# Kernel optimization log

Measured on AMD Instinct MI355X. Metric: run time of the kernel, lower is better.

Reference implementation:

```python
import jax, jax.numpy as jnp
import numpy as np

N_HEAD = 16
WINDOW = 128
CAUSAL = False


def setup_inputs() -> dict:
    key = jax.random.key(0)
    ks = jax.random.split(key, 5)
    B, T, D = 1, 4096, 1024
    x = jax.random.normal(ks[0], (B, T, D), dtype=jnp.float32)
    w_in = jax.random.normal(ks[1], (3 * D, D), dtype=jnp.float32) * 0.02
    b_in = jax.random.normal(ks[2], (3 * D,), dtype=jnp.float32) * 0.02
    w_out = jax.random.normal(ks[3], (D, D), dtype=jnp.float32) * 0.02
    b_out = jax.random.normal(ks[4], (D,), dtype=jnp.float32) * 0.02
    return {"x": x, "w_in": w_in, "b_in": b_in, "w_out": w_out, "b_out": b_out}


def _window_attention(x, w_in, b_in, w_out, b_out):
    B, T, D = x.shape
    H = N_HEAD
    hd = D // H
    scale = 1.0 / jnp.sqrt(jnp.float32(hd))

    # fused in-projection, as in torch nn.MultiheadAttention (y = x @ W^T + b)
    qkv = jnp.einsum('btd,ed->bte', x, w_in) + b_in  # (B, T, 3D)
    q, k, v = jnp.split(qkv, 3, axis=-1)
    # (B, H, T, hd)
    q = q.reshape(B, T, H, hd).transpose(0, 2, 1, 3)
    k = k.reshape(B, T, H, hd).transpose(0, 2, 1, 3)
    v = v.reshape(B, T, H, hd).transpose(0, 2, 1, 3)

    scores = jnp.einsum('bhqd,bhkd->bhqk', q, k) * scale  # (B, H, T, T)

    idx = jnp.arange(T)
    diff = idx[:, None] - idx[None, :]
    if CAUSAL:
        allowed = (diff >= 0) & (diff <= WINDOW)
    else:
        allowed = jnp.abs(diff) <= WINDOW
    NEG = jnp.float32(-1e30)
    scores = jnp.where(allowed[None, None, :, :], scores, NEG)

    attn = jax.nn.softmax(scores, axis=-1)
    ctx = jnp.einsum('bhqk,bhkd->bhqd', attn, v)  # (B, H, T, hd)
    ctx = ctx.transpose(0, 2, 1, 3).reshape(B, T, D)
    out = jnp.einsum('btd,ed->bte', ctx, w_out) + b_out
    return x + out  # residual, as in the module


def reference(x, w_in, b_in, w_out, b_out):
    return _window_attention(x, w_in, b_in, w_out, b_out)
```

## Files before the change

### kernel.cpp

```cpp
#include <hip/hip_runtime.h>

#define T_SEQ 4096
#define DMODEL 1024
#define NHEAD 16
#define HDIM 64
#define WIN 128

typedef __attribute__((ext_vector_type(8))) short bf16x8;
typedef __attribute__((ext_vector_type(4))) float f32x4;
typedef __attribute__((ext_vector_type(4))) unsigned short u16x4;

__device__ __forceinline__ unsigned short f2bf(float f) {
  unsigned int u = __builtin_bit_cast(unsigned int, f);
  return (unsigned short)((u + 0x7fffu + ((u >> 16) & 1u)) >> 16);
}

__device__ __forceinline__ void gload_lds16(const unsigned short* g,
                                            unsigned short* l) {
  __builtin_amdgcn_global_load_lds(
      (const __attribute__((address_space(1))) void*)g,
      (__attribute__((address_space(3))) void*)l, 16, 0, 0);
}

__global__ void convert_all(const float* __restrict__ x,
                            const float* __restrict__ w_in,
                            const float* __restrict__ w_out,
                            unsigned short* __restrict__ x_bf,
                            unsigned short* __restrict__ w_in_bf,
                            unsigned short* __restrict__ w_out_bf) {
  int stride = gridDim.x * blockDim.x;
  int t0 = blockIdx.x * blockDim.x + threadIdx.x;
#define CVT(SRC, DST, N4)                                          \
  for (int i = t0; i < (N4); i += stride) {                        \
    float4 v = reinterpret_cast<const float4*>(SRC)[i];            \
    u16x4 o;                                                       \
    o.x = f2bf(v.x); o.y = f2bf(v.y); o.z = f2bf(v.z); o.w = f2bf(v.w); \
    reinterpret_cast<u16x4*>(DST)[i] = o;                          \
  }
  CVT(x, x_bf, T_SEQ * DMODEL / 4)
  CVT(w_in, w_in_bf, 3 * DMODEL * DMODEL / 4)
  CVT(w_out, w_out_bf, DMODEL * DMODEL / 4)
#undef CVT
}

template <int EPI, int BM, int BN>
__device__ __forceinline__ void gemm_body(
    const unsigned short* __restrict__ A,
    const unsigned short* __restrict__ B,
    const float* __restrict__ bias,
    unsigned short* __restrict__ q_buf,
    unsigned short* __restrict__ k_buf,
    unsigned short* __restrict__ vt_buf,
    const float* __restrict__ x_res,
    float* __restrict__ out) {
  const int K = DMODEL;
  constexpr int NT = DMODEL / 64;
  constexpr int SM = BM / 2, SN = BN / 2;
  constexpr int MR = SM / 16, NR = SN / 16;
  constexpr int AL = BM / 32, BL = BN / 32;
  __shared__ __align__(16) unsigned short As[2 * BM * 64];
  __shared__ __align__(16) unsigned short Bs[2 * BN * 64];

  int tid = threadIdx.x;
  int lane = tid & 63, wave = tid >> 6;
  int wr = wave >> 1, wc = wave & 1;
  int lo = lane & 15, hi = lane >> 4;
  int t0 = blockIdx.y * BM, e0 = blockIdx.x * BN;

  f32x4 acc[MR][NR];
#pragma unroll
  for (int m = 0; m < MR; ++m)
#pragma unroll
    for (int n = 0; n < NR; ++n) acc[m][n] = (f32x4){0.f, 0.f, 0.f, 0.f};

  int c8 = (tid & 7) ^ ((tid >> 3) & 7);
  int srow = tid >> 3;
  const unsigned short* AbaseG = A + (size_t)(t0 + srow) * K + c8 * 8;
  const unsigned short* BbaseG = B + (size_t)(e0 + srow) * K + c8 * 8;
  unsigned short* ldsAu = As + wave * 512;
  unsigned short* ldsBu = Bs + wave * 512;

  auto stage = [&](int tt) {
    int k0 = tt * 64;
    int ab = (tt & 1) * (BM * 64);
    int bb = (tt & 1) * (BN * 64);
#pragma unroll
    for (int l = 0; l < AL; ++l)
      gload_lds16(AbaseG + (size_t)l * 32 * K + k0, ldsAu + l * 2048 + ab);
#pragma unroll
    for (int l = 0; l < BL; ++l)
      gload_lds16(BbaseG + (size_t)l * 32 * K + k0, ldsBu + l * 2048 + bb);
  };

  stage(0);
  asm volatile("s_waitcnt vmcnt(0) lgkmcnt(0)\n\ts_barrier" ::: "memory");

  for (int t = 0; t < NT; ++t) {
    if (t + 1 < NT) stage(t + 1);
    const unsigned short* Ab = As + (t & 1) * (BM * 64);
    const unsigned short* Bb = Bs + (t & 1) * (BN * 64);
    bf16x8 af[MR][2], bfr[NR][2];
#pragma unroll
    for (int m = 0; m < MR; ++m) {
      int row = wr * SM + m * 16 + lo;
#pragma unroll
      for (int ks = 0; ks < 2; ++ks)
        af[m][ks] = *reinterpret_cast<const bf16x8*>(
            &Ab[row * 64 + (((ks << 2) + hi) ^ (row & 7)) * 8]);
    }
#pragma unroll
    for (int n = 0; n < NR; ++n) {
      int row = wc * SN + n * 16 + lo;
#pragma unroll
      for (int ks = 0; ks < 2; ++ks)
        bfr[n][ks] = *reinterpret_cast<const bf16x8*>(
            &Bb[row * 64 + (((ks << 2) + hi) ^ (row & 7)) * 8]);
    }
#pragma unroll
    for (int ks = 0; ks < 2; ++ks)
#pragma unroll
      for (int m = 0; m < MR; ++m)
#pragma unroll
        for (int n = 0; n < NR; ++n)
          acc[m][n] = __builtin_amdgcn_mfma_f32_16x16x32_bf16(af[m][ks], bfr[n][ks],
                                                              acc[m][n], 0, 0, 0);
    asm volatile("s_waitcnt vmcnt(0) lgkmcnt(0)\n\ts_barrier" ::: "memory");
  }

  int t0w = t0 + wr * SM;
  int e0w = e0 + wc * SN;
#pragma unroll
  for (int m = 0; m < MR; ++m) {
#pragma unroll
    for (int n = 0; n < NR; ++n) {
      int e = e0w + n * 16 + lo;
      float bv = bias[e];
      if (EPI == 0) {
        int part = e >> 10;
        int h = (e >> 6) & 15;
        int d = e & 63;
        if (part == 2) {
          int t = t0w + m * 16 + hi * 4;
          u16x4 pk;
          pk.x = f2bf(acc[m][n][0] + bv);
          pk.y = f2bf(acc[m][n][1] + bv);
          pk.z = f2bf(acc[m][n][2] + bv);
          pk.w = f2bf(acc[m][n][3] + bv);
          *reinterpret_cast<u16x4*>(&vt_buf[((size_t)(h * HDIM + d)) * T_SEQ + t]) = pk;
        } else {
          unsigned short* dst = (part == 0) ? q_buf : k_buf;
#pragma unroll
          for (int jj = 0; jj < 4; ++jj) {
            int t = t0w + m * 16 + hi * 4 + jj;
            dst[((size_t)h * T_SEQ + t) * HDIM + d] = f2bf(acc[m][n][jj] + bv);
          }
        }
      } else {
#pragma unroll
        for (int jj = 0; jj < 4; ++jj) {
          int t = t0w + m * 16 + hi * 4 + jj;
          size_t idxo = (size_t)t * DMODEL + e;
          out[idxo] = acc[m][n][jj] + bv + x_res[idxo];
        }
      }
    }
  }
}

__global__ __launch_bounds__(256) void qkv_gemm(
    const unsigned short* __restrict__ A, const unsigned short* __restrict__ B,
    const float* __restrict__ bias, unsigned short* __restrict__ q_buf,
    unsigned short* __restrict__ k_buf, unsigned short* __restrict__ vt_buf) {
  gemm_body<0, 128, 192>(A, B, bias, q_buf, k_buf, vt_buf, nullptr, nullptr);
}

__global__ __launch_bounds__(256) void out_gemm(
    const unsigned short* __restrict__ A, const unsigned short* __restrict__ B,
    const float* __restrict__ bias, const float* __restrict__ x_res,
    float* __restrict__ out) {
  gemm_body<1, 128, 64>(A, B, bias, nullptr, nullptr, nullptr, x_res, out);
}

__global__ __launch_bounds__(256) void win_attn(
    const unsigned short* __restrict__ q_buf,
    const unsigned short* __restrict__ k_buf,
    const unsigned short* __restrict__ vt_buf,
    unsigned short* __restrict__ ctx) {
  __shared__ __align__(16) unsigned short p_lds[4][2][16 * 72];
  int tid = threadIdx.x;
  int wave = tid >> 6;
  int lane = tid & 63;
  int lo = lane & 15, hi = lane >> 4;

  int id = blockIdx.x;
  int sw = (id & 7) * (512 / 8) + (id >> 3);
  int job = sw * 4 + wave;
  int h = job >> 7;
  int q0 = (job & 127) * 32;
  const float SC = 0.18033688011112042f;

  bf16x8 aq[2][2];
#pragma unroll
  for (int u = 0; u < 2; ++u) {
    const unsigned short* qrow =
        q_buf + ((size_t)h * T_SEQ + q0 + u * 16 + lo) * HDIM + hi * 8;
    aq[u][0] = *reinterpret_cast<const bf16x8*>(qrow);
    aq[u][1] = *reinterpret_cast<const bf16x8*>(qrow + 32);
  }

  float L[2][4] = {{0.f, 0.f, 0.f, 0.f}, {0.f, 0.f, 0.f, 0.f}};
  f32x4 o[2][4];
#pragma unroll
  for (int u = 0; u < 2; ++u)
#pragma unroll
    for (int n = 0; n < 4; ++n) o[u][n] = (f32x4){0.f, 0.f, 0.f, 0.f};

  int jstart = q0 - WIN; if (jstart < 0) jstart = 0;
  int jend = q0 + 32 + WIN; if (jend > T_SEQ) jend = T_SEQ;

  for (int j0 = jstart; j0 < jend; j0 += 64) {
    bf16x8 kc[4][2];
#pragma unroll
    for (int c = 0; c < 4; ++c) {
      int krow = j0 + c * 16 + lo;
      if (krow > T_SEQ - 1) krow = T_SEQ - 1;
      const unsigned short* kp = k_buf + ((size_t)h * T_SEQ + krow) * HDIM + hi * 8;
      kc[c][0] = *reinterpret_cast<const bf16x8*>(kp);
      kc[c][1] = *reinterpret_cast<const bf16x8*>(kp + 32);
    }
    bf16x8 vc[4][2];
#pragma unroll
    for (int n = 0; n < 4; ++n) {
      const unsigned short* vp =
          vt_buf + ((size_t)(h * HDIM + n * 16 + lo)) * T_SEQ + j0 + hi * 8;
      vc[n][0] = *reinterpret_cast<const bf16x8*>(vp);
      vc[n][1] = *reinterpret_cast<const bf16x8*>(vp + 32);
    }
#pragma unroll
    for (int u = 0; u < 2; ++u) {
      f32x4 z[4];
      __builtin_amdgcn_s_setprio(1);
#pragma unroll
      for (int c = 0; c < 4; ++c) {
        z[c] = (f32x4){0.f, 0.f, 0.f, 0.f};
        z[c] = __builtin_amdgcn_mfma_f32_16x16x32_bf16(aq[u][0], kc[c][0], z[c], 0, 0, 0);
        z[c] = __builtin_amdgcn_mfma_f32_16x16x32_bf16(aq[u][1], kc[c][1], z[c], 0, 0, 0);
      }
      __builtin_amdgcn_s_setprio(0);
#pragma unroll
      for (int c = 0; c < 4; ++c) {
        int kj = j0 + c * 16 + lo;
#pragma unroll
        for (int jq = 0; jq < 4; ++jq) {
          int q = q0 + u * 16 + hi * 4 + jq;
          bool ok = (q - kj <= WIN) && (kj - q <= WIN);
          float p = ok ? __builtin_amdgcn_exp2f(z[c][jq] * SC) : 0.f;
          L[u][jq] += p;
          p_lds[wave][u][(hi * 4 + jq) * 72 + c * 16 + lo] = f2bf(p);
        }
      }
    }
    bf16x8 pa[2][2];
#pragma unroll
    for (int u = 0; u < 2; ++u) {
      pa[u][0] = *reinterpret_cast<const bf16x8*>(&p_lds[wave][u][lo * 72 + hi * 8]);
      pa[u][1] = *reinterpret_cast<const bf16x8*>(&p_lds[wave][u][lo * 72 + 32 + hi * 8]);
    }
    __builtin_amdgcn_s_setprio(1);
#pragma unroll
    for (int n = 0; n < 4; ++n) {
#pragma unroll
      for (int u = 0; u < 2; ++u) {
        o[u][n] = __builtin_amdgcn_mfma_f32_16x16x32_bf16(pa[u][0], vc[n][0], o[u][n], 0, 0, 0);
        o[u][n] = __builtin_amdgcn_mfma_f32_16x16x32_bf16(pa[u][1], vc[n][1], o[u][n], 0, 0, 0);
      }
    }
    __builtin_amdgcn_s_setprio(0);
  }
#pragma unroll
  for (int u = 0; u < 2; ++u)
#pragma unroll
    for (int jq = 0; jq < 4; ++jq) {
#pragma unroll
      for (int w = 1; w < 16; w <<= 1) L[u][jq] += __shfl_xor(L[u][jq], w, 64);
    }
#pragma unroll
  for (int u = 0; u < 2; ++u)
#pragma unroll
    for (int jq = 0; jq < 4; ++jq) {
      int t = q0 + u * 16 + hi * 4 + jq;
      float inv = 1.f / L[u][jq];
#pragma unroll
      for (int n = 0; n < 4; ++n)
        ctx[(size_t)t * DMODEL + h * HDIM + n * 16 + lo] = f2bf(o[u][n][jq] * inv);
    }
}

extern "C" void kernel_launch(void* const* d_in, const int* in_sizes, int n_in,
                              void* d_out, int out_size, void* d_ws, size_t ws_size,
                              hipStream_t stream) {
  const float* x = (const float*)d_in[0];
  const float* w_in = (const float*)d_in[1];
  const float* b_in = (const float*)d_in[2];
  const float* w_out = (const float*)d_in[3];
  const float* b_out = (const float*)d_in[4];
  float* out = (float*)d_out;

  char* ws = (char*)d_ws;
  size_t off = 0;
  auto take = [&](size_t bytes) {
    char* p = ws + off;
    off += (bytes + 255) & ~(size_t)255;
    return p;
  };
  unsigned short* x_bf = (unsigned short*)take((size_t)T_SEQ * DMODEL * 2);
  unsigned short* w_in_bf = (unsigned short*)take((size_t)3 * DMODEL * DMODEL * 2);
  unsigned short* w_out_bf = (unsigned short*)take((size_t)DMODEL * DMODEL * 2);
  unsigned short* q_buf = (unsigned short*)take((size_t)T_SEQ * DMODEL * 2);
  unsigned short* k_buf = (unsigned short*)take((size_t)T_SEQ * DMODEL * 2);
  unsigned short* vt_buf = (unsigned short*)take((size_t)T_SEQ * DMODEL * 2 + 16384);
  unsigned short* ctx = (unsigned short*)take((size_t)T_SEQ * DMODEL * 2);

  convert_all<<<2048, 256, 0, stream>>>(x, w_in, w_out, x_bf, w_in_bf, w_out_bf);

  dim3 g1(3 * DMODEL / 192, T_SEQ / 128);
  qkv_gemm<<<g1, 256, 0, stream>>>(x_bf, w_in_bf, b_in, q_buf, k_buf, vt_buf);

  win_attn<<<512, 256, 0, stream>>>(q_buf, k_buf, vt_buf, ctx);

  dim3 g2(DMODEL / 64, T_SEQ / 128);
  out_gemm<<<g2, 256, 0, stream>>>(ctx, w_out_bf, b_out, x, out);
}
```

Baseline: 91.55 us.

## Widen window-attention query tile to 64 and narrow key step to 32

Each wave now handles 64 queries instead of 32, and keys are stepped 32 at a time instead of 64. The wider query tile reuses each K/V load across more queries and cuts the redundant out-of-window key work per query, since the key span per query drops from 320 to 320/64 per row. The grid is halved to 256 blocks, which lowers the number of resident waves on a 256-CU part and could leave CUs idle. Register pressure also rises from the larger accumulator set, and launch_bounds(256,1) is added to allow it.

```diff
diff --git a/kernel.cpp b/kernel.cpp
--- a/kernel.cpp
+++ b/kernel.cpp
@@ -181,74 +181,74 @@
   gemm_body<1, 128, 64>(A, B, bias, nullptr, nullptr, nullptr, x_res, out);
 }
 
-__global__ __launch_bounds__(256) void win_attn(
+__global__ __launch_bounds__(256, 1) void win_attn(
     const unsigned short* __restrict__ q_buf,
     const unsigned short* __restrict__ k_buf,
     const unsigned short* __restrict__ vt_buf,
     unsigned short* __restrict__ ctx) {
-  __shared__ __align__(16) unsigned short p_lds[4][2][16 * 72];
+  __shared__ __align__(16) unsigned short p_lds[4][4][16 * 40];
   int tid = threadIdx.x;
   int wave = tid >> 6;
   int lane = tid & 63;
   int lo = lane & 15, hi = lane >> 4;
 
   int id = blockIdx.x;
-  int sw = (id & 7) * (512 / 8) + (id >> 3);
+  int sw = (id & 7) * 32 + (id >> 3);
   int job = sw * 4 + wave;
-  int h = job >> 7;
-  int q0 = (job & 127) * 32;
+  int h = job >> 6;
+  int q0 = (job & 63) * 64;
   const float SC = 0.18033688011112042f;
 
-  bf16x8 aq[2][2];
-#pragma unroll
-  for (int u = 0; u < 2; ++u) {
+  bf16x8 aq[4][2];
+#pragma unroll
+  for (int u = 0; u < 4; ++u) {
     const unsigned short* qrow =
         q_buf + ((size_t)h * T_SEQ + q0 + u * 16 + lo) * HDIM + hi * 8;
     aq[u][0] = *reinterpret_cast<const bf16x8*>(qrow);
     aq[u][1] = *reinterpret_cast<const bf16x8*>(qrow + 32);
   }
 
-  float L[2][4] = {{0.f, 0.f, 0.f, 0.f}, {0.f, 0.f, 0.f, 0.f}};
-  f32x4 o[2][4];
-#pragma unroll
-  for (int u = 0; u < 2; ++u)
-#pragma unroll
-    for (int n = 0; n < 4; ++n) o[u][n] = (f32x4){0.f, 0.f, 0.f, 0.f};
+  float L[4][4];
+  f32x4 o[4][4];
+#pragma unroll
+  for (int u = 0; u < 4; ++u)
+#pragma unroll
+    for (int n = 0; n < 4; ++n) {
+      o[u][n] = (f32x4){0.f, 0.f, 0.f, 0.f};
+      L[u][n] = 0.f;
+    }
 
   int jstart = q0 - WIN; if (jstart < 0) jstart = 0;
-  int jend = q0 + 32 + WIN; if (jend > T_SEQ) jend = T_SEQ;
-
-  for (int j0 = jstart; j0 < jend; j0 += 64) {
-    bf16x8 kc[4][2];
-#pragma unroll
-    for (int c = 0; c < 4; ++c) {
+  int jend = q0 + 64 + WIN; if (jend > T_SEQ) jend = T_SEQ;
+
+  for (int j0 = jstart; j0 < jend; j0 += 32) {
+    bf16x8 kc[2][2];
+#pragma unroll
+    for (int c = 0; c < 2; ++c) {
       int krow = j0 + c * 16 + lo;
       if (krow > T_SEQ - 1) krow = T_SEQ - 1;
       const unsigned short* kp = k_buf + ((size_t)h * T_SEQ + krow) * HDIM + hi * 8;
       kc[c][0] = *reinterpret_cast<const bf16x8*>(kp);
       kc[c][1] = *reinterpret_cast<const bf16x8*>(kp + 32);
     }
-    bf16x8 vc[4][2];
-#pragma unroll
-    for (int n = 0; n < 4; ++n) {
-      const unsigned short* vp =
-          vt_buf + ((size_t)(h * HDIM + n * 16 + lo)) * T_SEQ + j0 + hi * 8;
-      vc[n][0] = *reinterpret_cast<const bf16x8*>(vp);
-      vc[n][1] = *reinterpret_cast<const bf16x8*>(vp + 32);
-    }
-#pragma unroll
-    for (int u = 0; u < 2; ++u) {
-      f32x4 z[4];
+    bf16x8 vc[4];
+#pragma unroll
+    for (int n = 0; n < 4; ++n)
+      vc[n] = *reinterpret_cast<const bf16x8*>(
+          vt_buf + ((size_t)(h * HDIM + n * 16 + lo)) * T_SEQ + j0 + hi * 8);
+#pragma unroll
+    for (int u = 0; u < 4; ++u) {
+      f32x4 z[2];
       __builtin_amdgcn_s_setprio(1);
 #pragma unroll
-      for (int c = 0; c < 4; ++c) {
+      for (int c = 0; c < 2; ++c) {
         z[c] = (f32x4){0.f, 0.f, 0.f, 0.f};
         z[c] = __builtin_amdgcn_mfma_f32_16x16x32_bf16(aq[u][0], kc[c][0], z[c], 0, 0, 0);
         z[c] = __builtin_amdgcn_mfma_f32_16x16x32_bf16(aq[u][1], kc[c][1], z[c], 0, 0, 0);
       }
       __builtin_amdgcn_s_setprio(0);
 #pragma unroll
-      for (int c = 0; c < 4; ++c) {
+      for (int c = 0; c < 2; ++c) {
         int kj = j0 + c * 16 + lo;
 #pragma unroll
         for (int jq = 0; jq < 4; ++jq) {
@@ -256,36 +256,31 @@
           bool ok = (q - kj <= WIN) && (kj - q <= WIN);
           float p = ok ? __builtin_amdgcn_exp2f(z[c][jq] * SC) : 0.f;
           L[u][jq] += p;
-          p_lds[wave][u][(hi * 4 + jq) * 72 + c * 16 + lo] = f2bf(p);
+          p_lds[wave][u][(hi * 4 + jq) * 40 + c * 16 + lo] = f2bf(p);
         }
       }
     }
-    bf16x8 pa[2][2];
-#pragma unroll
-    for (int u = 0; u < 2; ++u) {
-      pa[u][0] = *reinterpret_cast<const bf16x8*>(&p_lds[wave][u][lo * 72 + hi * 8]);
-      pa[u][1] = *reinterpret_cast<const bf16x8*>(&p_lds[wave][u][lo * 72 + 32 + hi * 8]);
-    }
+    bf16x8 pa[4];
+#pragma unroll
+    for (int u = 0; u < 4; ++u)
+      pa[u] = *reinterpret_cast<const bf16x8*>(&p_lds[wave][u][lo * 40 + hi * 8]);
     __builtin_amdgcn_s_setprio(1);
 #pragma unroll
-    for (int n = 0; n < 4; ++n) {
-#pragma unroll
-      for (int u = 0; u < 2; ++u) {
-        o[u][n] = __builtin_amdgcn_mfma_f32_16x16x32_bf16(pa[u][0], vc[n][0], o[u][n], 0, 0, 0);
-        o[u][n] = __builtin_amdgcn_mfma_f32_16x16x32_bf16(pa[u][1], vc[n][1], o[u][n], 0, 0, 0);
-      }
-    }
+    for (int n = 0; n < 4; ++n)
+#pragma unroll
+      for (int u = 0; u < 4; ++u)
+        o[u][n] = __builtin_amdgcn_mfma_f32_16x16x32_bf16(pa[u], vc[n], o[u][n], 0, 0, 0);
     __builtin_amdgcn_s_setprio(0);
   }
 #pragma unroll
-  for (int u = 0; u < 2; ++u)
+  for (int u = 0; u < 4; ++u)
 #pragma unroll
     for (int jq = 0; jq < 4; ++jq) {
 #pragma unroll
       for (int w = 1; w < 16; w <<= 1) L[u][jq] += __shfl_xor(L[u][jq], w, 64);
     }
 #pragma unroll
-  for (int u = 0; u < 2; ++u)
+  for (int u = 0; u < 4; ++u)
 #pragma unroll
     for (int jq = 0; jq < 4; ++jq) {
       int t = q0 + u * 16 + hi * 4 + jq;
@@ -318,7 +313,7 @@
   unsigned short* w_out_bf = (unsigned short*)take((size_t)DMODEL * DMODEL * 2);
   unsigned short* q_buf = (unsigned short*)take((size_t)T_SEQ * DMODEL * 2);
   unsigned short* k_buf = (unsigned short*)take((size_t)T_SEQ * DMODEL * 2);
-  unsigned short* vt_buf = (unsigned short*)take((size_t)T_SEQ * DMODEL * 2 + 16384);
+  unsigned short* vt_buf = (unsigned short*)take((size_t)T_SEQ * DMODEL * 2 + 8192);
   unsigned short* ctx = (unsigned short*)take((size_t)T_SEQ * DMODEL * 2);
 
   convert_all<<<2048, 256, 0, stream>>>(x, w_in, w_out, x_bf, w_in_bf, w_out_bf);
@@ -326,7 +321,7 @@
   dim3 g1(3 * DMODEL / 192, T_SEQ / 128);
   qkv_gemm<<<g1, 256, 0, stream>>>(x_bf, w_in_bf, b_in, q_buf, k_buf, vt_buf);
 
-  win_attn<<<512, 256, 0, stream>>>(q_buf, k_buf, vt_buf, ctx);
+  win_attn<<<256, 256, 0, stream>>>(q_buf, k_buf, vt_buf, ctx);
 
   dim3 g2(DMODEL / 64, T_SEQ / 128);
   out_gemm<<<g2, 256, 0, stream>>>(ctx, w_out_bf, b_out, x, out);
```

Result: faster. 87.90 us, median of 2 (-4.0%).
